# Optimization experiments

Hardware: AMD Instinct MI355X
Metric: run time of the kernel (lower is better)

Reference implementation:

```python
import jax, jax.numpy as jnp
import numpy as np

BN_EPS = 1e-5


def haar_dwt2(x):
    # pywt.dwt2(img,'haar'/'db1') -> cA,(cH,cV,cD) with Haar filters lo=[1,1]/sqrt2, hi=[1,-1]/sqrt2.
    # cA=(a+b+c+d)/2, cH('da')=(a+b-c-d)/2, cV('ad')=(a-b+c-d)/2, cD=(a-b-c+d)/2
    # where a=x[2i,2j], b=x[2i,2j+1], c=x[2i+1,2j], d=x[2i+1,2j+1].
    B, C, H, W = x.shape
    xr = x.reshape(B, C, H // 2, 2, W // 2, 2)
    a = xr[:, :, :, 0, :, 0]
    b = xr[:, :, :, 0, :, 1]
    c = xr[:, :, :, 1, :, 0]
    d = xr[:, :, :, 1, :, 1]
    ll = (a + b + c + d) * 0.5
    lh = (a + b - c - d) * 0.5
    hl = (a - b + c - d) * 0.5
    hh = (a - b - c + d) * 0.5
    # interleave per input channel: [LL, LH, HL, HH] -> [B, 4C, H/2, W/2]
    return jnp.stack([ll, lh, hl, hh], axis=2).reshape(B, C * 4, H // 2, W // 2)


def conv_transpose2d(x, w, b):
    # torch ConvTranspose2d(k=4, s=2, p=1); w: [Cin, Cout, 4, 4] (torch layout)
    wk = jnp.flip(w, (-2, -1)).transpose(1, 0, 2, 3)  # [Cout, Cin, 4, 4]
    y = jax.lax.conv_general_dilated(
        x, wk, window_strides=(1, 1), padding=((2, 2), (2, 2)),
        lhs_dilation=(2, 2), dimension_numbers=('NCHW', 'OIHW', 'NCHW'))
    return y + b[None, :, None, None]


def bn_relu(x, g, beta, m, v):
    inv = g * jax.lax.rsqrt(v + BN_EPS)
    return jax.nn.relu((x - m[None, :, None, None]) * inv[None, :, None, None]
                       + beta[None, :, None, None])


def setup_inputs() -> dict:
    key = jax.random.key(0)
    ks = jax.random.split(key, 8)
    Cin, emb_dim = 3, 96
    half = emb_dim // 2  # 48
    B, H, W = 16, 256, 256
    x = jax.random.normal(ks[0], (B, Cin, H, W), dtype=jnp.float32)

    def convT_params(k, cin, cout):
        k1, k2 = jax.random.split(k)
        fan = float(cin * 16)
        w = jax.random.normal(k1, (cin, cout, 4, 4), dtype=jnp.float32) / np.sqrt(fan)
        b = jax.random.normal(k2, (cout,), dtype=jnp.float32) * 0.01
        return w, b

    def bn_params(k, c):
        k1, k2, k3 = jax.random.split(k, 3)
        g = 1.0 + 0.1 * jax.random.normal(k1, (c,), dtype=jnp.float32)
        beta = 0.1 * jax.random.normal(k2, (c,), dtype=jnp.float32)
        m = 0.1 * jax.random.normal(k3, (c,), dtype=jnp.float32)
        v = jnp.ones((c,), dtype=jnp.float32)
        return g, beta, m, v

    w1, b1 = convT_params(ks[1], 4 * Cin, half)
    g1, beta1, m1, v1 = bn_params(ks[2], half)
    w2a, b2a = convT_params(ks[3], 16 * Cin, half)
    g2a, beta2a, m2a, v2a = bn_params(ks[4], half)
    w2b, b2b = convT_params(ks[5], half, half)
    g2b, beta2b, m2b, v2b = bn_params(ks[6], half)

    return dict(x=x, w1=w1, b1=b1, g1=g1, beta1=beta1, m1=m1, v1=v1,
                w2a=w2a, b2a=b2a, g2a=g2a, beta2a=beta2a, m2a=m2a, v2a=v2a,
                w2b=w2b, b2b=b2b, g2b=g2b, beta2b=beta2b, m2b=m2b, v2b=v2b)


def reference(x, w1, b1, g1, beta1, m1, v1,
              w2a, b2a, g2a, beta2a, m2a, v2a,
              w2b, b2b, g2b, beta2b, m2b, v2b):
    x_l1 = haar_dwt2(x)                                  # [B, 4Cin, H/2, W/2]
    out = bn_relu(conv_transpose2d(x_l1, w1, b1), g1, beta1, m1, v1)   # [B, half, H, W]
    x_l2 = haar_dwt2(x_l1)                               # [B, 16Cin, H/4, W/4]
    out2 = bn_relu(conv_transpose2d(x_l2, w2a, b2a), g2a, beta2a, m2a, v2a)
    out2 = bn_relu(conv_transpose2d(out2, w2b, b2b), g2b, beta2b, m2b, v2b)  # [B, half, H, W]
    return jnp.concatenate([out, out2], axis=1)          # [B, emb_dim, H, W]
```

## Files before the change

kernel.cpp:

```cpp
#include <hip/hip_runtime.h>

typedef short s16x8 __attribute__((ext_vector_type(8)));
typedef float f32x4 __attribute__((ext_vector_type(4)));
typedef unsigned short u16;

#define BN_EPS 1e-5f

__device__ __forceinline__ u16 f2bf(float f) {
  union { float f; unsigned u; } v; v.f = f;
  unsigned r = (v.u + 0x7fffu + ((v.u >> 16) & 1u)) >> 16;
  return (u16)r;
}
__device__ __forceinline__ float bf2f(u16 u) {
  union { unsigned u; float f; } v; v.u = ((unsigned)u) << 16; return v.f;
}

__global__ __launch_bounds__(256) void dwt_fused_kernel(
    const float* __restrict__ x, u16* __restrict__ xl1, u16* __restrict__ xl2)
{
  int idx = blockIdx.x * 256 + threadIdx.x;
  int w4 = idx & 63; int t = idx >> 6;
  int h4 = t & 63; t >>= 6;
  int c = t % 3; int b = t / 3;
  const float* p = x + (((long)(b * 3 + c) * 256 + 4 * h4) * 256 + 4 * w4);
  float4 r[4];
  r[0] = *(const float4*)p;
  r[1] = *(const float4*)(p + 256);
  r[2] = *(const float4*)(p + 512);
  r[3] = *(const float4*)(p + 768);
  float rows[4][4] = {{r[0].x, r[0].y, r[0].z, r[0].w},
                      {r[1].x, r[1].y, r[1].z, r[1].w},
                      {r[2].x, r[2].y, r[2].z, r[2].w},
                      {r[3].x, r[3].y, r[3].z, r[3].w}};
  float sb[4][2][2];
  #pragma unroll
  for (int qy = 0; qy < 2; ++qy)
    #pragma unroll
    for (int qx = 0; qx < 2; ++qx) {
      float a = rows[2 * qy][2 * qx],     bb = rows[2 * qy][2 * qx + 1];
      float cc = rows[2 * qy + 1][2 * qx], dd = rows[2 * qy + 1][2 * qx + 1];
      sb[0][qy][qx] = (a + bb + cc + dd) * 0.5f;
      sb[1][qy][qx] = (a + bb - cc - dd) * 0.5f;
      sb[2][qy][qx] = (a - bb + cc - dd) * 0.5f;
      sb[3][qy][qx] = (a - bb - cc + dd) * 0.5f;
    }
  #pragma unroll
  for (int s = 0; s < 4; ++s)
    #pragma unroll
    for (int qy = 0; qy < 2; ++qy) {
      unsigned pk = (unsigned)f2bf(sb[s][qy][0]) | ((unsigned)f2bf(sb[s][qy][1]) << 16);
      *(unsigned*)&xl1[(((long)(b * 12 + 4 * c + s) * 128) + 2 * h4 + qy) * 128 + 2 * w4] = pk;
    }
  #pragma unroll
  for (int s = 0; s < 4; ++s) {
    float a = sb[s][0][0], bb = sb[s][0][1], cc = sb[s][1][0], dd = sb[s][1][1];
    float o[4] = {(a + bb + cc + dd) * 0.5f, (a + bb - cc - dd) * 0.5f,
                  (a - bb + cc - dd) * 0.5f, (a - bb - cc + dd) * 0.5f};
    #pragma unroll
    for (int s2 = 0; s2 < 4; ++s2)
      xl2[(((long)(b * 48 + (4 * c + s) * 4 + s2) * 64) + h4) * 64 + w4] = f2bf(o[s2]);
  }
}

__device__ void setup_one(
    const float* __restrict__ w, const float* __restrict__ bias,
    const float* __restrict__ g, const float* __restrict__ be,
    const float* __restrict__ mu, const float* __restrict__ var,
    u16* __restrict__ Bp, float* __restrict__ bnp,
    int CIN, int CIP, int KSTEPS, int e)
{
  if (e < 48) {
    float iv = g[e] * rsqrtf(var[e] + BN_EPS);
    bnp[e] = iv;
    bnp[48 + e] = (bias[e] - mu[e]) * iv + be[e];
  }
  int total = 4 * KSTEPS * 1536;
  if (e >= total) return;
  int j = e & 7;
  int l = (e >> 3) & 63;
  int nt = (e >> 9) % 3;
  int sp = e / 1536;
  int s = sp % KSTEPS;
  int p = sp / KSTEPS;
  int py = p >> 1, px = p & 1;
  int n = nt * 16 + (l & 15);
  int k = s * 32 + (l >> 4) * 8 + j;
  int tap = k / CIP, ci = k % CIP;
  int kh = 2 * (tap >> 1) + 1 - py;
  int kw = 2 * (tap & 1) + 1 - px;
  float v = (ci < CIN) ? w[((ci * 48 + n) * 4 + kh) * 4 + kw] : 0.f;
  Bp[e] = f2bf(v);
}

__global__ __launch_bounds__(256) void setup_all_kernel(
    const float* w1, const float* b1, const float* g1, const float* be1,
    const float* m1, const float* v1, u16* Bp1, float* bnp1,
    const float* w2a, const float* b2a, const float* g2a, const float* be2a,
    const float* m2a, const float* v2a, u16* Bp2a, float* bnp2a,
    const float* w2b, const float* b2b, const float* g2b, const float* be2b,
    const float* m2b, const float* v2b, u16* Bp2b, float* bnp2b)
{
  int e = blockIdx.x * 256 + threadIdx.x;
  if (blockIdx.y == 0)      setup_one(w1, b1, g1, be1, m1, v1, Bp1, bnp1, 12, 16, 2, e);
  else if (blockIdx.y == 1) setup_one(w2a, b2a, g2a, be2a, m2a, v2a, Bp2a, bnp2a, 48, 48, 6, e);
  else                      setup_one(w2b, b2b, g2b, be2b, m2b, v2b, Bp2b, bnp2b, 48, 48, 6, e);
}

template<int CIN, int CIP, int HIN, int WIN, bool OBF16>
__global__ __launch_bounds__(256, 2) void convt_mfma(
    const u16* __restrict__ in,
    const u16* __restrict__ Bp,
    const float* __restrict__ bnp,
    void* __restrict__ outv, int outc, int obase)
{
  constexpr int KSTEPS = CIP / 8;
  constexpr int ITX = 66, ITY = 6;
  constexpr int HOUT = 2 * HIN, WOUT = 2 * WIN;
  __shared__ __align__(16) u16 in_lds[ITX * ITY * CIP];
  __shared__ __align__(16) float out_lds[32 * 2 * 128];

  const int tid = threadIdx.x;
  const int n = blockIdx.z;
  const int qY0 = blockIdx.y * 4;
  const int qX0 = blockIdx.x * 64;

  {
    constexpr int NTASK = CIP * ITY * 8;
    for (int t = tid; t < NTASK; t += 256) {
      int seg = t & 7;
      int rowid = t >> 3;
      int ci = rowid / ITY;
      int y = rowid - ci * ITY;
      int ih = qY0 - 1 + y;
      bool rowok = (CIP == CIN || ci < CIN) && ((unsigned)ih < (unsigned)HIN);
      const u16* gsrc = in + (((long)n * CIN + ci) * HIN + ih) * WIN + qX0 + 8 * seg;
      s16x8 v = {0, 0, 0, 0, 0, 0, 0, 0};
      if (rowok) v = *(const s16x8*)gsrc;
      int base_yx = y * ITX;
      #pragma unroll
      for (int j = 0; j < 8; ++j) {
        int xx = 1 + 8 * seg + j;
        int rot = 8 * ((xx >> 2) & 3);
        if (rot >= CIP) rot -= CIP;
        int cr = ci + rot;
        if (cr >= CIP) cr -= CIP;
        in_lds[(base_yx + xx) * CIP + cr] = (u16)v[j];
      }
      if (seg == 0 || seg == 7) {
        int xh = (seg == 0) ? 0 : 65;
        int iwh = qX0 - 1 + xh;
        u16 hv = 0;
        if (rowok && (unsigned)iwh < (unsigned)WIN) hv = gsrc[(seg == 0) ? -1 : 8];
        int rot = 8 * ((xh >> 2) & 3);
        if (rot >= CIP) rot -= CIP;
        int cr = ci + rot;
        if (cr >= CIP) cr -= CIP;
        in_lds[(base_yx + xh) * CIP + cr] = hv;
      }
    }
  }

  const int wid = tid >> 6, lane = tid & 63;
  const int py = wid >> 1, px = wid & 1;
  const int g = lane >> 4, qx = lane & 15;

  s16x8 bf[KSTEPS][3];
  const s16x8* bpp = (const s16x8*)Bp + (wid * KSTEPS * 3) * 64 + lane;
  #pragma unroll
  for (int s = 0; s < KSTEPS; ++s)
    #pragma unroll
    for (int nt = 0; nt < 3; ++nt)
      bf[s][nt] = bpp[(s * 3 + nt) * 64];

  float4 inv4[3], sh4[3];
  #pragma unroll
  for (int nt = 0; nt < 3; ++nt) {
    inv4[nt] = *(const float4*)&bnp[nt * 16 + 4 * g];
    sh4[nt]  = *(const float4*)&bnp[48 + nt * 16 + 4 * g];
  }

  int abase[KSTEPS];
  #pragma unroll
  for (int s = 0; s < KSTEPS; ++s) {
    int k0 = s * 32 + g * 8;
    int tap = k0 / CIP, ci0 = k0 - tap * CIP;
    int ty = tap >> 1, tx = tap & 1;
    int y = 1 + py - ty;
    int xx = qx + 1 + px - tx;
    int rot = 8 * ((xx >> 2) & 3);
    if (rot >= CIP) rot -= CIP;
    int cr = ci0 + rot;
    if (cr >= CIP) cr -= CIP;
    abase[s] = (y * ITX + xx) * CIP + cr;
  }

  __syncthreads();

  for (int mc = 0; mc < 4; ++mc) {
    f32x4 acc[4][3];
    #pragma unroll
    for (int mt = 0; mt < 4; ++mt)
      #pragma unroll
      for (int nt = 0; nt < 3; ++nt)
        acc[mt][nt] = f32x4{0.f, 0.f, 0.f, 0.f};

    #pragma unroll
    for (int s = 0; s < KSTEPS; ++s) {
      #pragma unroll
      for (int mt = 0; mt < 4; ++mt) {
        s16x8 a = *(const s16x8*)&in_lds[abase[s] + (mc * ITX + mt * 16) * CIP];
        #pragma unroll
        for (int nt = 0; nt < 3; ++nt)
          acc[mt][nt] = __builtin_amdgcn_mfma_f32_16x16x32_bf16(
              bf[s][nt], a, acc[mt][nt], 0, 0, 0);
      }
    }

    #pragma unroll
    for (int sc = 0; sc < 2; ++sc) {
      const int ntlo = (sc == 0) ? 0 : 2;
      const int ntn  = (sc == 0) ? 2 : 1;
      const int coBase = ntlo * 16;
      __syncthreads();
      #pragma unroll
      for (int ntl = 0; ntl < 2; ++ntl) {
        if (ntl < ntn) {
          const int nt = ntlo + ntl;
          #pragma unroll
          for (int mt = 0; mt < 4; ++mt) {
            #pragma unroll
            for (int r = 0; r < 4; ++r) {
              const int co_rel = ntl * 16 + 4 * g + r;
              float iv = ((const float*)&inv4[nt])[r];
              float sv = ((const float*)&sh4[nt])[r];
              float val = fmaxf(acc[mt][nt][r] * iv + sv, 0.f);
              out_lds[(co_rel * 2 + py) * 128 + 2 * (mt * 16 + qx) + px] = val;
            }
          }
        }
      }
      __syncthreads();
      const int nIter = ntn * 4;
      #pragma unroll
      for (int u = 0; u < 8; ++u) {
        if (u < nIter) {
          int e = u * 256 + tid;
          int ow4 = e & 31, row = e >> 5;
          int co_l = coBase + (row >> 1), ohp = row & 1;
          f32x4 vv = *(const f32x4*)&out_lds[row * 128 + 4 * ow4];
          long off = (((long)(n * outc + obase + co_l) * HOUT + 2 * (qY0 + mc) + ohp) * WOUT)
                     + 2 * qX0 + 4 * ow4;
          if (OBF16) {
            unsigned lo = (unsigned)f2bf(vv.x) | ((unsigned)f2bf(vv.y) << 16);
            unsigned hi = (unsigned)f2bf(vv.z) | ((unsigned)f2bf(vv.w) << 16);
            uint2 pk; pk.x = lo; pk.y = hi;
            *(uint2*)((u16*)outv + off) = pk;
          } else {
            __builtin_nontemporal_store(vv, (f32x4*)((float*)outv + off));
          }
        }
      }
    }
  }
}

extern "C" void kernel_launch(void* const* d_in, const int* in_sizes, int n_in,
                              void* d_out, int out_size, void* d_ws, size_t ws_size,
                              hipStream_t stream) {
  const float* x    = (const float*)d_in[0];
  const float* w1   = (const float*)d_in[1];
  const float* b1   = (const float*)d_in[2];
  const float* g1   = (const float*)d_in[3];
  const float* be1  = (const float*)d_in[4];
  const float* m1   = (const float*)d_in[5];
  const float* v1   = (const float*)d_in[6];
  const float* w2a  = (const float*)d_in[7];
  const float* b2a  = (const float*)d_in[8];
  const float* g2a  = (const float*)d_in[9];
  const float* be2a = (const float*)d_in[10];
  const float* m2a  = (const float*)d_in[11];
  const float* v2a  = (const float*)d_in[12];
  const float* w2b  = (const float*)d_in[13];
  const float* b2b  = (const float*)d_in[14];
  const float* g2b  = (const float*)d_in[15];
  const float* be2b = (const float*)d_in[16];
  const float* m2b  = (const float*)d_in[17];
  const float* v2b  = (const float*)d_in[18];

  float* out = (float*)d_out;
  char* ws = (char*)d_ws;
  u16* xl1  = (u16*)ws;
  u16* xl2  = (u16*)(ws + 6291456);
  u16* o2a  = (u16*)(ws + 12582912);
  u16* Bp1  = (u16*)(ws + 37748736);
  u16* Bp2a = (u16*)(ws + 37773312);
  u16* Bp2b = (u16*)(ws + 37847040);
  float* bnp1  = (float*)(ws + 37920768);
  float* bnp2a = (float*)(ws + 37921152);
  float* bnp2b = (float*)(ws + 37921536);

  setup_all_kernel<<<dim3(144, 3), 256, 0, stream>>>(
      w1, b1, g1, be1, m1, v1, Bp1, bnp1,
      w2a, b2a, g2a, be2a, m2a, v2a, Bp2a, bnp2a,
      w2b, b2b, g2b, be2b, m2b, v2b, Bp2b, bnp2b);

  dwt_fused_kernel<<<768, 256, 0, stream>>>(x, xl1, xl2);

  convt_mfma<12, 16, 128, 128, false><<<dim3(2, 32, 16), 256, 0, stream>>>(
      xl1, Bp1, bnp1, out, 96, 0);
  convt_mfma<48, 48, 64, 64, true><<<dim3(1, 16, 16), 256, 0, stream>>>(
      xl2, Bp2a, bnp2a, o2a, 48, 0);
  convt_mfma<48, 48, 128, 128, false><<<dim3(2, 32, 16), 256, 0, stream>>>(
      o2a, Bp2b, bnp2b, out, 96, 48);
}
```

Before: 130.9 us.

## Merge setup and DWT kernels, halve conv tile width, raise occupancy

Folds the weight/BN setup kernel and the DWT kernel into one launch, which saves one launch and lets both kinds of blocks run at the same time. The transposed-conv tile shrinks from 64 to 32 input columns, which cuts LDS use and accumulator registers. Launch bounds go from 2 to 4 blocks per SM, and the grid doubles along x. B fragments are now loaded from global memory inside the k-loop instead of being held in registers. This trades register pressure for repeated global or cache reads, and adds more halo overhead per tile.

```diff
diff --git a/kernel.cpp b/kernel.cpp
--- a/kernel.cpp
+++ b/kernel.cpp
@@ -10,56 +10,6 @@
   union { float f; unsigned u; } v; v.f = f;
   unsigned r = (v.u + 0x7fffu + ((v.u >> 16) & 1u)) >> 16;
   return (u16)r;
-}
-__device__ __forceinline__ float bf2f(u16 u) {
-  union { unsigned u; float f; } v; v.u = ((unsigned)u) << 16; return v.f;
-}
-
-__global__ __launch_bounds__(256) void dwt_fused_kernel(
-    const float* __restrict__ x, u16* __restrict__ xl1, u16* __restrict__ xl2)
-{
-  int idx = blockIdx.x * 256 + threadIdx.x;
-  int w4 = idx & 63; int t = idx >> 6;
-  int h4 = t & 63; t >>= 6;
-  int c = t % 3; int b = t / 3;
-  const float* p = x + (((long)(b * 3 + c) * 256 + 4 * h4) * 256 + 4 * w4);
-  float4 r[4];
-  r[0] = *(const float4*)p;
-  r[1] = *(const float4*)(p + 256);
-  r[2] = *(const float4*)(p + 512);
-  r[3] = *(const float4*)(p + 768);
-  float rows[4][4] = {{r[0].x, r[0].y, r[0].z, r[0].w},
-                      {r[1].x, r[1].y, r[1].z, r[1].w},
-                      {r[2].x, r[2].y, r[2].z, r[2].w},
-                      {r[3].x, r[3].y, r[3].z, r[3].w}};
-  float sb[4][2][2];
-  #pragma unroll
-  for (int qy = 0; qy < 2; ++qy)
-    #pragma unroll
-    for (int qx = 0; qx < 2; ++qx) {
-      float a = rows[2 * qy][2 * qx],     bb = rows[2 * qy][2 * qx + 1];
-      float cc = rows[2 * qy + 1][2 * qx], dd = rows[2 * qy + 1][2 * qx + 1];
-      sb[0][qy][qx] = (a + bb + cc + dd) * 0.5f;
-      sb[1][qy][qx] = (a + bb - cc - dd) * 0.5f;
-      sb[2][qy][qx] = (a - bb + cc - dd) * 0.5f;
-      sb[3][qy][qx] = (a - bb - cc + dd) * 0.5f;
-    }
-  #pragma unroll
-  for (int s = 0; s < 4; ++s)
-    #pragma unroll
-    for (int qy = 0; qy < 2; ++qy) {
-      unsigned pk = (unsigned)f2bf(sb[s][qy][0]) | ((unsigned)f2bf(sb[s][qy][1]) << 16);
-      *(unsigned*)&xl1[(((long)(b * 12 + 4 * c + s) * 128) + 2 * h4 + qy) * 128 + 2 * w4] = pk;
-    }
-  #pragma unroll
-  for (int s = 0; s < 4; ++s) {
-    float a = sb[s][0][0], bb = sb[s][0][1], cc = sb[s][1][0], dd = sb[s][1][1];
-    float o[4] = {(a + bb + cc + dd) * 0.5f, (a + bb - cc - dd) * 0.5f,
-                  (a - bb + cc - dd) * 0.5f, (a - bb - cc + dd) * 0.5f};
-    #pragma unroll
-    for (int s2 = 0; s2 < 4; ++s2)
-      xl2[(((long)(b * 48 + (4 * c + s) * 4 + s2) * 64) + h4) * 64 + w4] = f2bf(o[s2]);
-  }
 }
 
 __device__ void setup_one(
@@ -92,7 +42,8 @@
   Bp[e] = f2bf(v);
 }
 
-__global__ __launch_bounds__(256) void setup_all_kernel(
+__global__ __launch_bounds__(256) void prep_kernel(
+    const float* __restrict__ x, u16* __restrict__ xl1, u16* __restrict__ xl2,
     const float* w1, const float* b1, const float* g1, const float* be1,
     const float* m1, const float* v1, u16* Bp1, float* bnp1,
     const float* w2a, const float* b2a, const float* g2a, const float* be2a,
@@ -100,35 +51,79 @@
     const float* w2b, const float* b2b, const float* g2b, const float* be2b,
     const float* m2b, const float* v2b, u16* Bp2b, float* bnp2b)
 {
-  int e = blockIdx.x * 256 + threadIdx.x;
-  if (blockIdx.y == 0)      setup_one(w1, b1, g1, be1, m1, v1, Bp1, bnp1, 12, 16, 2, e);
-  else if (blockIdx.y == 1) setup_one(w2a, b2a, g2a, be2a, m2a, v2a, Bp2a, bnp2a, 48, 48, 6, e);
-  else                      setup_one(w2b, b2b, g2b, be2b, m2b, v2b, Bp2b, bnp2b, 48, 48, 6, e);
+  if (blockIdx.x >= 768) {
+    int sub = blockIdx.x - 768;
+    int which = sub / 144;
+    int e = (sub % 144) * 256 + threadIdx.x;
+    if (which == 0)      setup_one(w1, b1, g1, be1, m1, v1, Bp1, bnp1, 12, 16, 2, e);
+    else if (which == 1) setup_one(w2a, b2a, g2a, be2a, m2a, v2a, Bp2a, bnp2a, 48, 48, 6, e);
+    else                 setup_one(w2b, b2b, g2b, be2b, m2b, v2b, Bp2b, bnp2b, 48, 48, 6, e);
+    return;
+  }
+  int idx = blockIdx.x * 256 + threadIdx.x;
+  int w4 = idx & 63; int t = idx >> 6;
+  int h4 = t & 63; t >>= 6;
+  int c = t % 3; int b = t / 3;
+  const float* p = x + (((long)(b * 3 + c) * 256 + 4 * h4) * 256 + 4 * w4);
+  float4 r0 = *(const float4*)p;
+  float4 r1 = *(const float4*)(p + 256);
+  float4 r2 = *(const float4*)(p + 512);
+  float4 r3 = *(const float4*)(p + 768);
+  float rows[4][4] = {{r0.x, r0.y, r0.z, r0.w}, {r1.x, r1.y, r1.z, r1.w},
+                      {r2.x, r2.y, r2.z, r2.w}, {r3.x, r3.y, r3.z, r3.w}};
+  float sb[4][2][2];
+  #pragma unroll
+  for (int qy = 0; qy < 2; ++qy)
+    #pragma unroll
+    for (int qx = 0; qx < 2; ++qx) {
+      float a = rows[2 * qy][2 * qx],      bb = rows[2 * qy][2 * qx + 1];
+      float cc = rows[2 * qy + 1][2 * qx], dd = rows[2 * qy + 1][2 * qx + 1];
+      sb[0][qy][qx] = (a + bb + cc + dd) * 0.5f;
+      sb[1][qy][qx] = (a + bb - cc - dd) * 0.5f;
+      sb[2][qy][qx] = (a - bb + cc - dd) * 0.5f;
+      sb[3][qy][qx] = (a - bb - cc + dd) * 0.5f;
+    }
+  #pragma unroll
+  for (int s = 0; s < 4; ++s)
+    #pragma unroll
+    for (int qy = 0; qy < 2; ++qy) {
+      unsigned pk = (unsigned)f2bf(sb[s][qy][0]) | ((unsigned)f2bf(sb[s][qy][1]) << 16);
+      *(unsigned*)&xl1[(((long)(b * 12 + 4 * c + s) * 128) + 2 * h4 + qy) * 128 + 2 * w4] = pk;
+    }
+  #pragma unroll
+  for (int s = 0; s < 4; ++s) {
+    float a = sb[s][0][0], bb = sb[s][0][1], cc = sb[s][1][0], dd = sb[s][1][1];
+    float o[4] = {(a + bb + cc + dd) * 0.5f, (a + bb - cc - dd) * 0.5f,
+                  (a - bb + cc - dd) * 0.5f, (a - bb - cc + dd) * 0.5f};
+    #pragma unroll
+    for (int s2 = 0; s2 < 4; ++s2)
+      xl2[(((long)(b * 48 + (4 * c + s) * 4 + s2) * 64) + h4) * 64 + w4] = f2bf(o[s2]);
+  }
 }
 
 template<int CIN, int CIP, int HIN, int WIN, bool OBF16>
-__global__ __launch_bounds__(256, 2) void convt_mfma(
+__global__ __launch_bounds__(256, 4) void convt_mfma(
     const u16* __restrict__ in,
     const u16* __restrict__ Bp,
     const float* __restrict__ bnp,
     void* __restrict__ outv, int outc, int obase)
 {
   constexpr int KSTEPS = CIP / 8;
-  constexpr int ITX = 66, ITY = 6;
+  constexpr int ITX = 34, ITY = 6;
   constexpr int HOUT = 2 * HIN, WOUT = 2 * WIN;
   __shared__ __align__(16) u16 in_lds[ITX * ITY * CIP];
-  __shared__ __align__(16) float out_lds[32 * 2 * 128];
+  __shared__ __align__(16) float out_lds[32 * 2 * 64];
 
   const int tid = threadIdx.x;
   const int n = blockIdx.z;
   const int qY0 = blockIdx.y * 4;
-  const int qX0 = blockIdx.x * 64;
+  const int qX0 = blockIdx.x * 32;
 
   {
-    constexpr int NTASK = CIP * ITY * 8;
+    constexpr int NTASK = CIP * ITY * 4;
     for (int t = tid; t < NTASK; t += 256) {
-      int seg = t & 7;
-      int rowid = t >> 3;
+      int seg = t & 3;
+      int rowid = t >> 2;
       int ci = rowid / ITY;
       int y = rowid - ci * ITY;
       int ih = qY0 - 1 + y;
@@ -146,8 +141,8 @@
         if (cr >= CIP) cr -= CIP;
         in_lds[(base_yx + xx) * CIP + cr] = (u16)v[j];
       }
-      if (seg == 0 || seg == 7) {
-        int xh = (seg == 0) ? 0 : 65;
+      if (seg == 0 || seg == 3) {
+        int xh = (seg == 0) ? 0 : 33;
         int iwh = qX0 - 1 + xh;
         u16 hv = 0;
         if (rowok && (unsigned)iwh < (unsigned)WIN) hv = gsrc[(seg == 0) ? -1 : 8];
@@ -164,13 +159,7 @@
   const int py = wid >> 1, px = wid & 1;
   const int g = lane >> 4, qx = lane & 15;
 
-  s16x8 bf[KSTEPS][3];
   const s16x8* bpp = (const s16x8*)Bp + (wid * KSTEPS * 3) * 64 + lane;
-  #pragma unroll
-  for (int s = 0; s < KSTEPS; ++s)
-    #pragma unroll
-    for (int nt = 0; nt < 3; ++nt)
-      bf[s][nt] = bpp[(s * 3 + nt) * 64];
 
   float4 inv4[3], sh4[3];
   #pragma unroll
@@ -197,22 +186,24 @@
   __syncthreads();
 
   for (int mc = 0; mc < 4; ++mc) {
-    f32x4 acc[4][3];
-    #pragma unroll
-    for (int mt = 0; mt < 4; ++mt)
+    f32x4 acc[2][3];
+    #pragma unroll
+    for (int mt = 0; mt < 2; ++mt)
       #pragma unroll
       for (int nt = 0; nt < 3; ++nt)
         acc[mt][nt] = f32x4{0.f, 0.f, 0.f, 0.f};
 
     #pragma unroll
     for (int s = 0; s < KSTEPS; ++s) {
-      #pragma unroll
-      for (int mt = 0; mt < 4; ++mt) {
+      s16x8 bf0 = bpp[(s * 3 + 0) * 64];
+      s16x8 bf1 = bpp[(s * 3 + 1) * 64];
+      s16x8 bf2 = bpp[(s * 3 + 2) * 64];
+      #pragma unroll
+      for (int mt = 0; mt < 2; ++mt) {
         s16x8 a = *(const s16x8*)&in_lds[abase[s] + (mc * ITX + mt * 16) * CIP];
-        #pragma unroll
-        for (int nt = 0; nt < 3; ++nt)
-          acc[mt][nt] = __builtin_amdgcn_mfma_f32_16x16x32_bf16(
-              bf[s][nt], a, acc[mt][nt], 0, 0, 0);
+        acc[mt][0] = __builtin_amdgcn_mfma_f32_16x16x32_bf16(bf0, a, acc[mt][0], 0, 0, 0);
+        acc[mt][1] = __builtin_amdgcn_mfma_f32_16x16x32_bf16(bf1, a, acc[mt][1], 0, 0, 0);
+        acc[mt][2] = __builtin_amdgcn_mfma_f32_16x16x32_bf16(bf2, a, acc[mt][2], 0, 0, 0);
       }
     }
 
@@ -227,27 +218,27 @@
         if (ntl < ntn) {
           const int nt = ntlo + ntl;
           #pragma unroll
-          for (int mt = 0; mt < 4; ++mt) {
+          for (int mt = 0; mt < 2; ++mt) {
             #pragma unroll
             for (int r = 0; r < 4; ++r) {
               const int co_rel = ntl * 16 + 4 * g + r;
               float iv = ((const float*)&inv4[nt])[r];
               float sv = ((const float*)&sh4[nt])[r];
               float val = fmaxf(acc[mt][nt][r] * iv + sv, 0.f);
-              out_lds[(co_rel * 2 + py) * 128 + 2 * (mt * 16 + qx) + px] = val;
+              out_lds[(co_rel * 2 + py) * 64 + 2 * (mt * 16 + qx) + px] = val;
             }
           }
         }
       }
       __syncthreads();
-      const int nIter = ntn * 4;
-      #pragma unroll
-      for (int u = 0; u < 8; ++u) {
+      const int nIter = ntn * 2;
+      #pragma unroll
+      for (int u = 0; u < 4; ++u) {
         if (u < nIter) {
           int e = u * 256 + tid;
-          int ow4 = e & 31, row = e >> 5;
+          int ow4 = e & 15, row = e >> 4;
           int co_l = coBase + (row >> 1), ohp = row & 1;
-          f32x4 vv = *(const f32x4*)&out_lds[row * 128 + 4 * ow4];
+          f32x4 vv = *(const f32x4*)&out_lds[row * 64 + 4 * ow4];
           long off = (((long)(n * outc + obase + co_l) * HOUT + 2 * (qY0 + mc) + ohp) * WOUT)
                      + 2 * qX0 + 4 * ow4;
           if (OBF16) {
@@ -299,17 +290,16 @@
   float* bnp2a = (float*)(ws + 37921152);
   float* bnp2b = (float*)(ws + 37921536);
 
-  setup_all_kernel<<<dim3(144, 3), 256, 0, stream>>>(
+  prep_kernel<<<1200, 256, 0, stream>>>(
+      x, xl1, xl2,
       w1, b1, g1, be1, m1, v1, Bp1, bnp1,
       w2a, b2a, g2a, be2a, m2a, v2a, Bp2a, bnp2a,
       w2b, b2b, g2b, be2b, m2b, v2b, Bp2b, bnp2b);
 
-  dwt_fused_kernel<<<768, 256, 0, stream>>>(x, xl1, xl2);
-
-  convt_mfma<12, 16, 128, 128, false><<<dim3(2, 32, 16), 256, 0, stream>>>(
+  convt_mfma<48, 48, 64, 64, true><<<dim3(2, 16, 16), 256, 0, stream>>>(
+      xl2, Bp2a, bnp2a, o2a, 48, 0);
+  convt_mfma<12, 16, 128, 128, false><<<dim3(4, 32, 16), 256, 0, stream>>>(
       xl1, Bp1, bnp1, out, 96, 0);
-  convt_mfma<48, 48, 64, 64, true><<<dim3(1, 16, 16), 256, 0, stream>>>(
-      xl2, Bp2a, bnp2a, o2a, 48, 0);
-  convt_mfma<48, 48, 128, 128, false><<<dim3(2, 32, 16), 256, 0, stream>>>(
+  convt_mfma<48, 48, 128, 128, false><<<dim3(4, 32, 16), 256, 0, stream>>>(
       o2a, Bp2b, bnp2b, out, 96, 48);
 }
```

Result: faster. 120.0 us (-8.3%).
